# Kernel tuning notes

Measured on AMD Instinct MI355X. Metric: run time of the kernel, lower is better.

Reference implementation:

```python
import jax, jax.numpy as jnp
import numpy as np

B, FG, ANT, D = 256, 4, 32, 1024   # batch, freq_groups, antennas, d_model
H, DK = 16, 64                      # n_heads, d_k; inner_dim = H*DK = 1024
INNER = H * DK


def setup_inputs() -> dict:
    key = jax.random.key(0)
    ks = jax.random.split(key, 17)
    s = 0.02
    inp = {"x": jax.random.normal(ks[0], (B, FG * ANT, D), dtype=jnp.float32)}
    names = ["ant_q", "ant_k", "ant_v", "ant_out", "freq_q", "freq_k", "freq_v", "freq_out"]
    for i, n in enumerate(names):
        # all layers are D->INNER or INNER->D; here D == INNER == 1024
        inp[n + "_w"] = jax.random.normal(ks[1 + 2 * i], (D, INNER), dtype=jnp.float32) * s
        inp[n + "_b"] = jnp.zeros((INNER,), dtype=jnp.float32)
    return inp


def _elu1(x):
    return jax.nn.elu(x) + 1.0


def _linear_attention(x, wq, bq, wk, bk, wv, bv):
    # x: (Baug, Lax, D)
    Baug, Lax, _ = x.shape
    Q = _elu1((x @ wq + bq).reshape(Baug, Lax, H, DK))
    K = _elu1((x @ wk + bk).reshape(Baug, Lax, H, DK))
    V = (x @ wv + bv).reshape(Baug, Lax, H, DK)
    KV = jnp.einsum('blhd,blhe->bhde', K, V)      # (Baug, H, DK, DK)
    out = jnp.einsum('blhd,bhde->blhe', Q, KV)    # (Baug, Lax, H, DK)
    return out.reshape(Baug, Lax, INNER)


def reference(x, ant_q_w, ant_q_b, ant_k_w, ant_k_b, ant_v_w, ant_v_b,
              ant_out_w, ant_out_b, freq_q_w, freq_q_b, freq_k_w, freq_k_b,
              freq_v_w, freq_v_b, freq_out_w, freq_out_b):
    # L == ANT*FG, no CLS token; dropout is identity (eval mode)
    grid_ant = x.reshape(B * FG, ANT, D)
    ant = _linear_attention(grid_ant, ant_q_w, ant_q_b, ant_k_w, ant_k_b, ant_v_w, ant_v_b)
    grid_ant = grid_ant + (ant @ ant_out_w + ant_out_b)
    # (B, FG, ANT, D) -> (B, ANT, FG, D)
    grid = grid_ant.reshape(B, FG, ANT, D).transpose(0, 2, 1, 3)
    grid_freq = grid.reshape(B * ANT, FG, D)
    frq = _linear_attention(grid_freq, freq_q_w, freq_q_b, freq_k_w, freq_k_b, freq_v_w, freq_v_b)
    grid_freq = grid_freq + (frq @ freq_out_w + freq_out_b)
    # back to (B, FG, ANT, D) -> (B, L, D)
    out = grid_freq.reshape(B, ANT, FG, D).transpose(0, 2, 1, 3).reshape(B, FG * ANT, D)
    return out
```

## Files before the change

kernel.cpp:

```cpp
#include <hip/hip_runtime.h>
#include <math.h>


#define MTOT 32768
#define DM 1024

using half8   = __attribute__((ext_vector_type(8))) _Float16;
using h2      = __attribute__((ext_vector_type(2))) _Float16;
using floatx4 = __attribute__((ext_vector_type(4))) float;

#define ACT_NONE 0
#define ACT_ELU1 1
#define REMAP_NONE 0
#define REMAP_A2F 1
#define REMAP_F2O 2

#define VMWAIT(n) asm volatile("s_waitcnt vmcnt(" #n ")" ::: "memory")
#define SBAR() do { __builtin_amdgcn_s_barrier(); \
                    __builtin_amdgcn_sched_barrier(0); } while (0)

__device__ __forceinline__ void gload16(const void* g, void* ldsp) {
  __builtin_amdgcn_global_load_lds(
      (const __attribute__((address_space(1))) unsigned int*)g,
      (__attribute__((address_space(3))) unsigned int*)ldsp, 16, 0, 0);
}

__device__ __forceinline__ float fdot2f(h2 a, h2 b, float c) {
#if __has_builtin(__builtin_amdgcn_fdot2)
  return __builtin_amdgcn_fdot2(a, b, c, false);
#else
  return fmaf((float)a[0], (float)b[0], fmaf((float)a[1], (float)b[1], c));
#endif
}

template<int ACT, int REMAP, bool RES, bool OF32, bool OF16>
__global__ __launch_bounds__(512, 4) void gemm_k(
    const _Float16* __restrict__ A, const _Float16* __restrict__ W,
    const float* __restrict__ bias, const _Float16* __restrict__ resid,
    float rs, float* __restrict__ Cf, _Float16* __restrict__ Ch,
    float sin_s, float sout_s)
{
  __shared__ __align__(16) char lds[73728];

  const int t = threadIdx.x, w = t >> 6, l = t & 63;
  const int bx = blockIdx.x;
  const int m0 = (((bx & 7) << 5) + (bx >> 3)) * 128;
  const int n0 = blockIdx.y * 256;
  const int lr = l & 15, ls = l >> 4;
  const int wrow = (w >> 2) * 64, wcol = (w & 3) * 64;

  const int v    = (t & 7) ^ ((t >> 3) & 7);
  const int arow = ((t >> 3) << 1) + (v >> 2);
  const int akh  = (v & 3) * 8;
  const int wloff = w * 1024;

  int aoff[4], boff[4];
#pragma unroll
  for (int m = 0; m < 4; ++m) {
    int ra = wrow + m * 16 + lr;
    aoff[m] = (ra >> 1) * 128 + ((((ra & 1) << 2 | ls) ^ ((ra >> 1) & 7)) << 4);
    int rb = wcol + m * 16 + lr;
    boff[m] = 8192 + (rb >> 1) * 128 +
              ((((rb & 1) << 2 | ls) ^ ((rb >> 1) & 7)) << 4);
  }

  floatx4 acc[4][4];
#pragma unroll
  for (int m = 0; m < 4; ++m)
#pragma unroll
    for (int n = 0; n < 4; ++n) acc[m][n] = (floatx4)0.f;

  auto stage = [&](int kt, int s) {
    const int kb = kt * 32;
    char* const sb = lds + s * 24576;
    gload16(A + (size_t)(m0 + arow) * DM + kb + akh, sb + wloff);
    gload16(W + (size_t)(n0 + arow) * DM + kb + akh, sb + 8192 + wloff);
    gload16(W + (size_t)(n0 + 128 + arow) * DM + kb + akh, sb + 16384 + wloff);
  };

  auto compute = [&](int s) {
    const char* sb = lds + s * 24576;
    half8 af[4], bf[4];
#pragma unroll
    for (int m = 0; m < 4; ++m) af[m] = *(const half8*)(sb + aoff[m]);
#pragma unroll
    for (int n = 0; n < 4; ++n) bf[n] = *(const half8*)(sb + boff[n]);
    __builtin_amdgcn_s_setprio(1);
#pragma unroll
    for (int m = 0; m < 4; ++m)
#pragma unroll
      for (int n = 0; n < 4; ++n)
        acc[m][n] =
            __builtin_amdgcn_mfma_f32_16x16x32_f16(af[m], bf[n], acc[m][n], 0, 0, 0);
    __builtin_amdgcn_s_setprio(0);
  };

  stage(0, 0);
  stage(1, 1);
  for (int t2 = 0; t2 < 30; ++t2) {
    stage(t2 + 2, (t2 + 2) % 3);
    VMWAIT(6);
    SBAR();
    compute(t2 % 3);
    SBAR();
  }
  VMWAIT(3); SBAR(); compute(0); SBAR();
  VMWAIT(0); SBAR(); compute(1);

  float bb[4];
#pragma unroll
  for (int n = 0; n < 4; ++n) bb[n] = bias[n0 + wcol + n * 16 + lr];

#pragma unroll
  for (int m = 0; m < 4; ++m)
#pragma unroll
    for (int n = 0; n < 4; ++n)
#pragma unroll
      for (int j = 0; j < 4; ++j) {
        int rt = wrow + m * 16 + ls * 4 + j;
        int ct = wcol + n * 16 + lr;
        float v2 = acc[m][n][j] * sin_s + bb[n];
        if (RES) v2 += rs * (float)resid[(size_t)(m0 + rt) * DM + n0 + ct];
        if (ACT == ACT_ELU1) v2 = (v2 > 0.f) ? (v2 + 1.f) : expf(v2);
        acc[m][n][j] = v2;
      }
  if (RES && REMAP != REMAP_NONE) __syncthreads();

#pragma unroll
  for (int m = 0; m < 4; ++m)
#pragma unroll
    for (int n = 0; n < 4; ++n)
#pragma unroll
      for (int j = 0; j < 4; ++j) {
        int rt = wrow + m * 16 + ls * 4 + j;
        int ct = wcol + n * 16 + lr;
        int mg = m0 + rt, ng = n0 + ct;
        int srw;
        if (REMAP == REMAP_NONE) {
          srw = mg;
        } else if (REMAP == REMAP_A2F) {
          int b = mg >> 7, fg = (mg >> 5) & 3, ant = mg & 31;
          srw = b * 128 + ant * 4 + fg;
        } else {
          int b = mg >> 7, ant = (mg >> 2) & 31, fg = mg & 3;
          srw = b * 128 + fg * 32 + ant;
        }
        float v2 = acc[m][n][j];
        if (OF32) Cf[(size_t)srw * DM + ng] = v2;
        if (OF16) Ch[(size_t)srw * DM + ng] = (_Float16)(v2 * sout_s);
      }
}

__global__ __launch_bounds__(256) void linattn32_k(
    _Float16* __restrict__ Q, const _Float16* __restrict__ K,
    const _Float16* __restrict__ V, float sout)
{
  __shared__ _Float16 Qs[32][64];
  __shared__ _Float16 Ks[32][64];
  __shared__ _Float16 Vs[32][64];
  __shared__ float Ss[32][33];

  const int g = blockIdx.x, h = blockIdx.y;
  const size_t base = (size_t)g * 32 * DM + h * 64;
  const int t = threadIdx.x;

  {
    const int row = t >> 3, ch = (t & 7) * 8;
    half8 q8 = *(const half8*)(Q + base + (size_t)row * DM + ch);
    half8 k8 = *(const half8*)(K + base + (size_t)row * DM + ch);
    half8 v8 = *(const half8*)(V + base + (size_t)row * DM + ch);
    *(half8*)&Qs[row][ch ^ ((row & 7) * 8)] = q8;
    *(half8*)&Ks[row][ch ^ (((row >> 2) & 7) * 8)] = k8;
    *(half8*)&Vs[row][ch] = v8;
  }
  __syncthreads();

  {
    const int tt = t >> 3, sg = t & 7;
    const int xq = (tt & 7) * 8, xk = sg * 8;
    float acc[4] = {};
#pragma unroll
    for (int jj = 0; jj < 32; ++jj) {
      h2 qq = *(const h2*)&Qs[tt][(2 * jj) ^ xq];
#pragma unroll
      for (int si = 0; si < 4; ++si) {
        h2 kk = *(const h2*)&Ks[sg * 4 + si][(2 * jj) ^ xk];
        acc[si] = fdot2f(qq, kk, acc[si]);
      }
    }
#pragma unroll
    for (int si = 0; si < 4; ++si) Ss[tt][sg * 4 + si] = acc[si];
  }
  __syncthreads();

  {
    const int tt = t >> 3, e0 = (t & 7) * 8;
    float o[8] = {};
#pragma unroll
    for (int s = 0; s < 32; ++s) {
      float sv = Ss[tt][s];
      half8 vv = *(const half8*)&Vs[s][e0];
#pragma unroll
      for (int e = 0; e < 8; ++e) o[e] = fmaf(sv, (float)vv[e], o[e]);
    }
    half8 r;
#pragma unroll
    for (int e = 0; e < 8; ++e) r[e] = (_Float16)(o[e] * sout);
    *(half8*)(Q + base + (size_t)tt * DM + e0) = r;
  }
}

__global__ __launch_bounds__(256) void linattn4_k(
    _Float16* __restrict__ Q, const _Float16* __restrict__ K,
    const _Float16* __restrict__ V, float sout)
{
  __shared__ _Float16 Qs[4][1024];
  __shared__ _Float16 Ks[4][1024];
  __shared__ _Float16 Vs[4][1024];
  __shared__ float Ss[16][4][5];

  const int g = blockIdx.x;
  const size_t base = (size_t)g * 4 * DM;
  const int t = threadIdx.x;

  {
    const int off = t * 16;
    const int row = off >> 10, col = off & 1023;
    const int h = col >> 6, d = col & 63, x = (h & 7) * 8;
    const int c0 = h * 64 + (d ^ x), c1 = h * 64 + ((d + 8) ^ x);
    half8 q0 = *(const half8*)(Q + base + off);
    half8 q1 = *(const half8*)(Q + base + off + 8);
    half8 k0 = *(const half8*)(K + base + off);
    half8 k1 = *(const half8*)(K + base + off + 8);
    half8 v0 = *(const half8*)(V + base + off);
    half8 v1 = *(const half8*)(V + base + off + 8);
    *(half8*)&Qs[row][c0] = q0; *(half8*)&Qs[row][c1] = q1;
    *(half8*)&Ks[row][c0] = k0; *(half8*)&Ks[row][c1] = k1;
    *(half8*)&Vs[row][c0] = v0; *(half8*)&Vs[row][c1] = v1;
  }
  __syncthreads();

  {
    const int h = t >> 4, tt = (t >> 2) & 3, s = t & 3;
    const int x = (h & 7) * 8;
    const _Float16* qp = &Qs[tt][h * 64];
    const _Float16* kp = &Ks[s][h * 64];
    float acc = 0.f;
#pragma unroll
    for (int jj = 0; jj < 32; ++jj) {
      int dd = (2 * jj) ^ x;
      acc = fdot2f(*(const h2*)(qp + dd), *(const h2*)(kp + dd), acc);
    }
    Ss[h][tt][s] = acc;
  }
  __syncthreads();

  {
    const int tt = t >> 6, cg = t & 63;
    const int h = cg >> 2, e0 = (cg & 3) * 16, x = (h & 7) * 8;
    const float* sp = Ss[h][tt];
    float o[16] = {};
#pragma unroll
    for (int s = 0; s < 4; ++s) {
      float sv = sp[s];
      half8 va = *(const half8*)&Vs[s][h * 64 + (e0 ^ x)];
      half8 vb = *(const half8*)&Vs[s][h * 64 + ((e0 + 8) ^ x)];
#pragma unroll
      for (int e = 0; e < 8; ++e) {
        o[e]     = fmaf(sv, (float)va[e], o[e]);
        o[e + 8] = fmaf(sv, (float)vb[e], o[e + 8]);
      }
    }
    half8 r0, r1;
#pragma unroll
    for (int e = 0; e < 8; ++e) {
      r0[e] = (_Float16)(o[e] * sout);
      r1[e] = (_Float16)(o[e + 8] * sout);
    }
    _Float16* dst = Q + base + (size_t)tt * DM + h * 64 + e0;
    *(half8*)dst = r0;
    *(half8*)(dst + 8) = r1;
  }
}

struct WPtrs { const float* p[8]; };

__global__ __launch_bounds__(256) void transpose_w8_k(
    WPtrs ws, _Float16* __restrict__ wt)
{
  __shared__ float tile[32][33];
  const float* W = ws.p[blockIdx.z];
  _Float16* Wt = wt + (size_t)DM * DM * blockIdx.z;
  const int tx = threadIdx.x & 31, ty = threadIdx.x >> 5;
  const int k0 = blockIdx.x * 32, n0 = blockIdx.y * 32;
#pragma unroll
  for (int r = 0; r < 4; ++r)
    tile[ty + r * 8][tx] = W[(size_t)(k0 + ty + r * 8) * DM + n0 + tx];
  __syncthreads();
#pragma unroll
  for (int r = 0; r < 4; ++r)
    Wt[(size_t)(n0 + ty + r * 8) * DM + k0 + tx] = (_Float16)tile[tx][ty + r * 8];
}

__global__ __launch_bounds__(256) void convf2h_k(
    const float* __restrict__ x, _Float16* __restrict__ xh, int n8)
{
  for (int i = blockIdx.x * blockDim.x + threadIdx.x; i < n8;
       i += gridDim.x * blockDim.x) {
    float4 a = ((const float4*)x)[i * 2];
    float4 b = ((const float4*)x)[i * 2 + 1];
    half8 h;
    h[0] = (_Float16)a.x; h[1] = (_Float16)a.y; h[2] = (_Float16)a.z; h[3] = (_Float16)a.w;
    h[4] = (_Float16)b.x; h[5] = (_Float16)b.y; h[6] = (_Float16)b.z; h[7] = (_Float16)b.w;
    ((half8*)xh)[i] = h;
  }
}

extern "C" void kernel_launch(void* const* d_in, const int* in_sizes, int n_in,
                              void* d_out, int out_size, void* d_ws, size_t ws_size,
                              hipStream_t stream)
{
  const float* x   = (const float*)d_in[0];
  WPtrs wp;
  for (int j = 0; j < 8; ++j) wp.p[j] = (const float*)d_in[1 + 2 * j];
  const float* aqb = (const float*)d_in[2];  const float* akb = (const float*)d_in[4];
  const float* avb = (const float*)d_in[6];  const float* aob = (const float*)d_in[8];
  const float* fqb = (const float*)d_in[10]; const float* fkb = (const float*)d_in[12];
  const float* fvb = (const float*)d_in[14]; const float* fob = (const float*)d_in[16];
  float* out = (float*)d_out;

  const size_t NE = (size_t)MTOT * DM;
  _Float16* xh = (_Float16*)d_ws;
  _Float16* Qh = xh + NE;
  _Float16* Kh = Qh + NE;
  _Float16* Vh = Kh + NE;
  _Float16* wt = Vh + NE;
  const size_t WSZ = (size_t)DM * DM;

  dim3 gg(MTOT / 128, DM / 256), gb(512), sb(256);

  convf2h_k<<<2048, sb, 0, stream>>>(x, xh, (int)(NE / 8));
  transpose_w8_k<<<dim3(32, 32, 8), sb, 0, stream>>>(wp, wt);

  const float S = 0.0625f;

  gemm_k<ACT_ELU1, REMAP_NONE, false, false, true><<<gg, gb, 0, stream>>>(
      xh, wt + WSZ * 0, aqb, nullptr, 0.f, nullptr, Qh, 1.f, 1.f);
  gemm_k<ACT_ELU1, REMAP_NONE, false, false, true><<<gg, gb, 0, stream>>>(
      xh, wt + WSZ * 1, akb, nullptr, 0.f, nullptr, Kh, 1.f, 1.f);
  gemm_k<ACT_NONE, REMAP_NONE, false, false, true><<<gg, gb, 0, stream>>>(
      xh, wt + WSZ * 2, avb, nullptr, 0.f, nullptr, Vh, 1.f, 1.f);
  linattn32_k<<<dim3(1024, 16), sb, 0, stream>>>(Qh, Kh, Vh, S);
  gemm_k<ACT_NONE, REMAP_A2F, true, false, true><<<gg, gb, 0, stream>>>(
      Qh, wt + WSZ * 3, aob, xh, 1.f, nullptr, xh, 16.f, S);

  gemm_k<ACT_ELU1, REMAP_NONE, false, false, true><<<gg, gb, 0, stream>>>(
      xh, wt + WSZ * 4, fqb, nullptr, 0.f, nullptr, Qh, 16.f, S);
  gemm_k<ACT_ELU1, REMAP_NONE, false, false, true><<<gg, gb, 0, stream>>>(
      xh, wt + WSZ * 5, fkb, nullptr, 0.f, nullptr, Kh, 16.f, S);
  gemm_k<ACT_NONE, REMAP_NONE, false, false, true><<<gg, gb, 0, stream>>>(
      xh, wt + WSZ * 6, fvb, nullptr, 0.f, nullptr, Vh, 16.f, S);
  linattn4_k<<<8192, sb, 0, stream>>>(Qh, Kh, Vh, S);
  gemm_k<ACT_NONE, REMAP_F2O, true, true, false><<<gg, gb, 0, stream>>>(
      Qh, wt + WSZ * 7, fob, xh, 16.f, out, nullptr, 65536.f, 1.f);
}
```

Measured before the change: 911.4 us.

## Enlarge GEMM tile to 256x256 with split-phase interleaved load/MFMA pipeline

Doubles the GEMM block tile in M from 128 to 256 rows, so each wave now accumulates an 8x4 grid of 16x16 MFMA tiles and the grid halves in M. Each K-step is split into two phases that interleave the global-to-LDS loads for A and W with the two halves of the MFMA work, using explicit barriers and lgkmcnt waits. The goal is more operand reuse per LDS byte and better overlap of memory traffic with compute. In exchange it uses more registers and LDS, drops occupancy to 2 blocks per CU, and leaves fewer blocks to fill the GPU.

Result: faster. 874.9 us (-4.0%).

```diff
diff --git a/kernel.cpp b/kernel.cpp
--- a/kernel.cpp
+++ b/kernel.cpp
@@ -16,7 +16,10 @@
 #define REMAP_F2O 2
 
 #define VMWAIT(n) asm volatile("s_waitcnt vmcnt(" #n ")" ::: "memory")
-#define SBAR() do { __builtin_amdgcn_s_barrier(); \
+#define LGKM0() do { asm volatile("s_waitcnt lgkmcnt(0)" ::: "memory"); \
+                     __builtin_amdgcn_sched_barrier(0); } while (0)
+#define SBAR() do { __builtin_amdgcn_sched_barrier(0); \
+                    __builtin_amdgcn_s_barrier(); \
                     __builtin_amdgcn_sched_barrier(0); } while (0)
 
 __device__ __forceinline__ void gload16(const void* g, void* ldsp) {
@@ -34,85 +37,132 @@
 }
 
 template<int ACT, int REMAP, bool RES, bool OF32, bool OF16>
-__global__ __launch_bounds__(512, 4) void gemm_k(
+__global__ __launch_bounds__(512, 2) void gemm_k(
     const _Float16* __restrict__ A, const _Float16* __restrict__ W,
     const float* __restrict__ bias, const _Float16* __restrict__ resid,
     float rs, float* __restrict__ Cf, _Float16* __restrict__ Ch,
     float sin_s, float sout_s)
 {
-  __shared__ __align__(16) char lds[73728];
+  __shared__ __align__(16) char lds[98304];
 
   const int t = threadIdx.x, w = t >> 6, l = t & 63;
   const int bx = blockIdx.x;
-  const int m0 = (((bx & 7) << 5) + (bx >> 3)) * 128;
+  const int m0 = (((bx & 7) << 4) + (bx >> 3)) * 256;
   const int n0 = blockIdx.y * 256;
   const int lr = l & 15, ls = l >> 4;
-  const int wrow = (w >> 2) * 64, wcol = (w & 3) * 64;
+  const int wrow = (w >> 2) * 128, wcol = (w & 3) * 64;
 
   const int v    = (t & 7) ^ ((t >> 3) & 7);
   const int arow = ((t >> 3) << 1) + (v >> 2);
   const int akh  = (v & 3) * 8;
   const int wloff = w * 1024;
 
-  int aoff[4], boff[4];
-#pragma unroll
-  for (int m = 0; m < 4; ++m) {
+  int aoff[8], boff[4];
+#pragma unroll
+  for (int m = 0; m < 8; ++m) {
     int ra = wrow + m * 16 + lr;
     aoff[m] = (ra >> 1) * 128 + ((((ra & 1) << 2 | ls) ^ ((ra >> 1) & 7)) << 4);
-    int rb = wcol + m * 16 + lr;
-    boff[m] = 8192 + (rb >> 1) * 128 +
+  }
+#pragma unroll
+  for (int n = 0; n < 4; ++n) {
+    int rb = wcol + n * 16 + lr;
+    boff[n] = 16384 + (rb >> 1) * 128 +
               ((((rb & 1) << 2 | ls) ^ ((rb >> 1) & 7)) << 4);
   }
 
-  floatx4 acc[4][4];
-#pragma unroll
-  for (int m = 0; m < 4; ++m)
+  floatx4 acc[8][4];
+#pragma unroll
+  for (int m = 0; m < 8; ++m)
 #pragma unroll
     for (int n = 0; n < 4; ++n) acc[m][n] = (floatx4)0.f;
 
-  auto stage = [&](int kt, int s) {
+  auto stage4 = [&](int kt, int s) {
     const int kb = kt * 32;
-    char* const sb = lds + s * 24576;
+    char* const sb = lds + s * 32768;
     gload16(A + (size_t)(m0 + arow) * DM + kb + akh, sb + wloff);
-    gload16(W + (size_t)(n0 + arow) * DM + kb + akh, sb + 8192 + wloff);
-    gload16(W + (size_t)(n0 + 128 + arow) * DM + kb + akh, sb + 16384 + wloff);
+    gload16(A + (size_t)(m0 + 128 + arow) * DM + kb + akh, sb + 8192 + wloff);
+    gload16(W + (size_t)(n0 + arow) * DM + kb + akh, sb + 16384 + wloff);
+    gload16(W + (size_t)(n0 + 128 + arow) * DM + kb + akh, sb + 24576 + wloff);
   };
 
-  auto compute = [&](int s) {
-    const char* sb = lds + s * 24576;
-    half8 af[4], bf[4];
+  auto tail_step = [&](const char* sb) {
+    half8 bf[4], af[4];
+#pragma unroll
+    for (int n = 0; n < 4; ++n) bf[n] = *(const half8*)(sb + boff[n]);
 #pragma unroll
     for (int m = 0; m < 4; ++m) af[m] = *(const half8*)(sb + aoff[m]);
-#pragma unroll
-    for (int n = 0; n < 4; ++n) bf[n] = *(const half8*)(sb + boff[n]);
+    SBAR(); LGKM0();
     __builtin_amdgcn_s_setprio(1);
 #pragma unroll
     for (int m = 0; m < 4; ++m)
 #pragma unroll
       for (int n = 0; n < 4; ++n)
-        acc[m][n] =
-            __builtin_amdgcn_mfma_f32_16x16x32_f16(af[m], bf[n], acc[m][n], 0, 0, 0);
+        acc[m][n] = __builtin_amdgcn_mfma_f32_16x16x32_f16(af[m], bf[n], acc[m][n], 0, 0, 0);
+    __builtin_amdgcn_s_setprio(0);
+    SBAR();
+#pragma unroll
+    for (int m = 0; m < 4; ++m) af[m] = *(const half8*)(sb + aoff[4 + m]);
+    SBAR(); LGKM0();
+    __builtin_amdgcn_s_setprio(1);
+#pragma unroll
+    for (int m = 0; m < 4; ++m)
+#pragma unroll
+      for (int n = 0; n < 4; ++n)
+        acc[4 + m][n] = __builtin_amdgcn_mfma_f32_16x16x32_f16(af[m], bf[n], acc[4 + m][n], 0, 0, 0);
     __builtin_amdgcn_s_setprio(0);
   };
 
-  stage(0, 0);
-  stage(1, 1);
+  stage4(0, 0);
+  stage4(1, 1);
+  VMWAIT(4);
+  SBAR();
+
   for (int t2 = 0; t2 < 30; ++t2) {
-    stage(t2 + 2, (t2 + 2) % 3);
-    VMWAIT(6);
+    const char* sb = lds + (t2 % 3) * 32768;
+    char* nb = lds + ((t2 + 2) % 3) * 32768;
+    const int kb = (t2 + 2) * 32;
+    half8 bf[4], af[4];
+#pragma unroll
+    for (int n = 0; n < 4; ++n) bf[n] = *(const half8*)(sb + boff[n]);
+#pragma unroll
+    for (int m = 0; m < 4; ++m) af[m] = *(const half8*)(sb + aoff[m]);
+    gload16(A + (size_t)(m0 + arow) * DM + kb + akh, nb + wloff);
+    gload16(A + (size_t)(m0 + 128 + arow) * DM + kb + akh, nb + 8192 + wloff);
+    SBAR(); LGKM0();
+    __builtin_amdgcn_s_setprio(1);
+#pragma unroll
+    for (int m = 0; m < 4; ++m)
+#pragma unroll
+      for (int n = 0; n < 4; ++n)
+        acc[m][n] = __builtin_amdgcn_mfma_f32_16x16x32_f16(af[m], bf[n], acc[m][n], 0, 0, 0);
+    __builtin_amdgcn_s_setprio(0);
     SBAR();
-    compute(t2 % 3);
+#pragma unroll
+    for (int m = 0; m < 4; ++m) af[m] = *(const half8*)(sb + aoff[4 + m]);
+    gload16(W + (size_t)(n0 + arow) * DM + kb + akh, nb + 16384 + wloff);
+    gload16(W + (size_t)(n0 + 128 + arow) * DM + kb + akh, nb + 24576 + wloff);
+    SBAR(); LGKM0();
+    __builtin_amdgcn_s_setprio(1);
+#pragma unroll
+    for (int m = 0; m < 4; ++m)
+#pragma unroll
+      for (int n = 0; n < 4; ++n)
+        acc[4 + m][n] = __builtin_amdgcn_mfma_f32_16x16x32_f16(af[m], bf[n], acc[4 + m][n], 0, 0, 0);
+    __builtin_amdgcn_s_setprio(0);
+    VMWAIT(4);
     SBAR();
   }
-  VMWAIT(3); SBAR(); compute(0); SBAR();
-  VMWAIT(0); SBAR(); compute(1);
+  tail_step(lds);
+  VMWAIT(0);
+  SBAR();
+  tail_step(lds + 32768);
 
   float bb[4];
 #pragma unroll
   for (int n = 0; n < 4; ++n) bb[n] = bias[n0 + wcol + n * 16 + lr];
 
 #pragma unroll
-  for (int m = 0; m < 4; ++m)
+  for (int m = 0; m < 8; ++m)
 #pragma unroll
     for (int n = 0; n < 4; ++n)
 #pragma unroll
@@ -127,7 +177,7 @@
   if (RES && REMAP != REMAP_NONE) __syncthreads();
 
 #pragma unroll
-  for (int m = 0; m < 4; ++m)
+  for (int m = 0; m < 8; ++m)
 #pragma unroll
     for (int n = 0; n < 4; ++n)
 #pragma unroll
@@ -337,7 +387,7 @@
   _Float16* wt = Vh + NE;
   const size_t WSZ = (size_t)DM * DM;
 
-  dim3 gg(MTOT / 128, DM / 256), gb(512), sb(256);
+  dim3 gg(MTOT / 256, DM / 256), gb(512), sb(256);
 
   convf2h_k<<<2048, sb, 0, stream>>>(x, xh, (int)(NE / 8));
   transpose_w8_k<<<dim3(32, 32, 8), sb, 0, stream>>>(wp, wt);
```
